# Kernel optimization log

Measured on AMD Instinct MI355X. Metric: run time of the kernel, lower is better.

## Reference

```python
import jax, jax.numpy as jnp
import numpy as np

N_NODES = 10000  # static number of graph nodes (segment count)


def setup_inputs() -> dict:
    key = jax.random.key(0)
    ks = jax.random.split(key, 7)
    B, N, DIN, DOUT, E = 2, N_NODES, 256, 256, 320000
    x = jax.random.normal(ks[0], (B, N, DIN), dtype=jnp.float32)
    W = jax.random.normal(ks[1], (DIN, DOUT), dtype=jnp.float32) * (1.0 / np.sqrt(DIN))
    loop_W = jax.random.normal(ks[2], (DIN, DOUT), dtype=jnp.float32) * (1.0 / np.sqrt(DIN))
    bias = jax.random.normal(ks[3], (DOUT,), dtype=jnp.float32) * 0.01
    edge_vals = jax.random.uniform(ks[4], (E,), dtype=jnp.float32)
    rows = jax.random.randint(ks[5], (E,), 0, N, dtype=jnp.int32)
    cols = jax.random.randint(ks[6], (E,), 0, N, dtype=jnp.int32)
    return {"x": x, "W": W, "loop_W": loop_W, "bias": bias,
            "edge_vals": edge_vals, "rows": rows, "cols": cols}


def reference(x, W, loop_W, bias, edge_vals, rows, cols):
    # Dense feature transforms: [b,n,din] @ [din,dout] -> [b,n,dout]
    support = jnp.einsum('bni,io->bno', x, W)
    support_loop = jnp.einsum('bni,io->bno', x, loop_W)
    # Sparse adjacency matmul (COO SpMM): out[r] += val_e * support[:, c_e, :]
    msgs = support[:, cols, :] * edge_vals[None, :, None]      # [b, E, dout]
    agg = jax.ops.segment_sum(
        jnp.swapaxes(msgs, 0, 1), rows, num_segments=N_NODES)   # [n, b, dout]
    agg = jnp.swapaxes(agg, 0, 1)                                # [b, n, dout]
    out = agg + support_loop + bias
    return jax.nn.relu(out)
```

## Files before the change

kernel.cpp:

```cpp
#include <hip/hip_runtime.h>
#include <hip/hip_bf16.h>


#define NN 10000
#define DK 256
#define DO 256
#define MT 20000
#define SCAN_T 256
#define SCAN_C 40

typedef short short8 __attribute__((ext_vector_type(8)));
typedef float f32x4 __attribute__((ext_vector_type(4)));

__device__ inline unsigned short f2bf(float f) {
    unsigned int u = __float_as_uint(f);
    u = (u + 0x7FFFu + ((u >> 16) & 1u)) >> 16;
    return (unsigned short)u;
}
__device__ inline float bf2f(unsigned short s) {
    return __uint_as_float(((unsigned int)s) << 16);
}

__global__ __launch_bounds__(256) void cvt_x(
    const float* __restrict__ X, unsigned short* __restrict__ Xb, int n8)
{
    const int i = blockIdx.x * 256 + threadIdx.x;
    if (i >= n8) return;
    const float4 a = ((const float4*)X)[2 * i];
    const float4 b = ((const float4*)X)[2 * i + 1];
    short8 o;
    o[0] = (short)f2bf(a.x); o[1] = (short)f2bf(a.y);
    o[2] = (short)f2bf(a.z); o[3] = (short)f2bf(a.w);
    o[4] = (short)f2bf(b.x); o[5] = (short)f2bf(b.y);
    o[6] = (short)f2bf(b.z); o[7] = (short)f2bf(b.w);
    *(short8*)&Xb[(size_t)i * 8] = o;
}

__global__ __launch_bounds__(256) void transpose_w(
    const float* __restrict__ W, const float* __restrict__ LW,
    unsigned short* __restrict__ Wt, unsigned short* __restrict__ LWt)
{
    __shared__ float tile[64][65];
    const float* src = blockIdx.z ? LW : W;
    unsigned short* dst = blockIdx.z ? LWt : Wt;
    const int k0 = blockIdx.x * 64, c0 = blockIdx.y * 64;
    #pragma unroll
    for (int it = 0; it < 16; ++it) {
        const int u = it * 256 + threadIdx.x;
        const int i = u >> 6, j = u & 63;
        tile[i][j] = src[(size_t)(k0 + i) * DO + c0 + j];
    }
    __syncthreads();
    #pragma unroll
    for (int it = 0; it < 16; ++it) {
        const int u = it * 256 + threadIdx.x;
        const int j = u >> 6, i = u & 63;
        dst[(size_t)(c0 + j) * DK + k0 + i] = f2bf(tile[i][j]);
    }
}

__global__ __launch_bounds__(256) void gemm_mfma(
    const unsigned short* __restrict__ Xb, const unsigned short* __restrict__ Wt,
    const unsigned short* __restrict__ LWt, const float* __restrict__ bias,
    unsigned short* __restrict__ sup, float* __restrict__ outv)
{
    __shared__ unsigned short As[8][128][8];
    __shared__ unsigned short Bs[8][128][8];
    const int t = threadIdx.x;
    const int wid = t >> 6, lane = t & 63;
    const int wm = wid >> 1, wn = wid & 1;
    const int m0 = blockIdx.x * 128;
    const int n0 = blockIdx.y * 128;
    const bool isLoop = (blockIdx.z != 0);
    const unsigned short* Bsrc = isLoop ? LWt : Wt;

    f32x4 acc[4][4];
    #pragma unroll
    for (int i = 0; i < 4; ++i)
        #pragma unroll
        for (int j = 0; j < 4; ++j)
            acc[i][j] = (f32x4){0.f, 0.f, 0.f, 0.f};

    for (int k0 = 0; k0 < DK; k0 += 64) {
        #pragma unroll
        for (int it = 0; it < 4; ++it) {
            const int u = it * 256 + t;
            const int row = u >> 3, kg = u & 7;
            const int grow = m0 + row;
            short8 v = (short8){0,0,0,0,0,0,0,0};
            if (grow < MT) v = *(const short8*)&Xb[(size_t)grow * DK + k0 + kg * 8];
            *(short8*)&As[kg][row ^ kg][0] = v;
        }
        #pragma unroll
        for (int it = 0; it < 4; ++it) {
            const int u = it * 256 + t;
            const int col = u >> 3, kg = u & 7;
            const short8 v = *(const short8*)&Bsrc[(size_t)(n0 + col) * DK + k0 + kg * 8];
            *(short8*)&Bs[kg][col ^ kg][0] = v;
        }
        __syncthreads();
        #pragma unroll
        for (int s = 0; s < 2; ++s) {
            const int kg = s * 4 + (lane >> 4);
            short8 af[4], bfv[4];
            #pragma unroll
            for (int i = 0; i < 4; ++i) {
                const int row = wm * 64 + i * 16 + (lane & 15);
                af[i] = *(const short8*)&As[kg][row ^ kg][0];
            }
            #pragma unroll
            for (int j = 0; j < 4; ++j) {
                const int col = wn * 64 + j * 16 + (lane & 15);
                bfv[j] = *(const short8*)&Bs[kg][col ^ kg][0];
            }
            #pragma unroll
            for (int i = 0; i < 4; ++i)
                #pragma unroll
                for (int j = 0; j < 4; ++j)
                    acc[i][j] = __builtin_amdgcn_mfma_f32_16x16x32_bf16(
                        af[i], bfv[j], acc[i][j], 0, 0, 0);
        }
        __syncthreads();
    }

    const int rbase = m0 + wm * 64;
    const int cbase = n0 + wn * 64;
    if (!isLoop) {
        #pragma unroll
        for (int i = 0; i < 4; ++i)
            #pragma unroll
            for (int q = 0; q < 4; ++q) {
                const int row = rbase + i * 16 + (lane >> 4) * 4 + q;
                if (row < MT) {
                    #pragma unroll
                    for (int j = 0; j < 4; ++j) {
                        const int col = cbase + j * 16 + (lane & 15);
                        sup[(size_t)row * DO + col] = f2bf(acc[i][j][q]);
                    }
                }
            }
    } else {
        #pragma unroll
        for (int i = 0; i < 4; ++i)
            #pragma unroll
            for (int q = 0; q < 4; ++q) {
                const int row = rbase + i * 16 + (lane >> 4) * 4 + q;
                if (row < MT) {
                    #pragma unroll
                    for (int j = 0; j < 4; ++j) {
                        const int col = cbase + j * 16 + (lane & 15);
                        outv[(size_t)row * DO + col] = acc[i][j][q] + bias[col];
                    }
                }
            }
    }
}

__global__ __launch_bounds__(256) void zero_counts(int* __restrict__ counts, int n)
{
    const int i = blockIdx.x * 256 + threadIdx.x;
    if (i < n) counts[i] = 0;
}

__global__ __launch_bounds__(256) void hist_rows(
    const int* __restrict__ rows, int* __restrict__ counts, int E)
{
    const int e = blockIdx.x * 256 + threadIdx.x;
    if (e < E) atomicAdd(&counts[rows[e]], 1);
}

__global__ __launch_bounds__(SCAN_T) void scan_rows(
    const int* __restrict__ counts, int* __restrict__ offsets,
    int* __restrict__ cursor)
{
    __shared__ int sums[SCAN_T];
    const int t = threadIdx.x;
    int local[SCAN_C];
    int s = 0;
    const int base = t * SCAN_C;
    #pragma unroll
    for (int i = 0; i < SCAN_C; ++i) {
        const int idx = base + i;
        const int c = (idx < NN) ? counts[idx] : 0;
        local[i] = s;
        s += c;
    }
    sums[t] = s;
    __syncthreads();
    for (int off = 1; off < SCAN_T; off <<= 1) {
        int u = (t >= off) ? sums[t - off] : 0;
        __syncthreads();
        sums[t] += u;
        __syncthreads();
    }
    const int excl = (t == 0) ? 0 : sums[t - 1];
    #pragma unroll
    for (int i = 0; i < SCAN_C; ++i) {
        const int idx = base + i;
        if (idx < NN) {
            const int o = excl + local[i];
            offsets[idx] = o;
            cursor[idx]  = o;
        }
    }
}

__global__ __launch_bounds__(256) void scatter_edges(
    const int* __restrict__ rows, const int* __restrict__ cols,
    const float* __restrict__ vals, int* __restrict__ cursor,
    float2* __restrict__ epack, int E)
{
    const int e = blockIdx.x * 256 + threadIdx.x;
    if (e >= E) return;
    const int p = atomicAdd(&cursor[rows[e]], 1);
    epack[p] = make_float2(__int_as_float(cols[e]), vals[e]);
}

__global__ __launch_bounds__(256) void agg_relu(
    const unsigned short* __restrict__ sup, const float2* __restrict__ epack,
    const int* __restrict__ offsets, const int* __restrict__ counts,
    float* __restrict__ outv)
{
    const int widx = (blockIdx.x * 256 + threadIdx.x) >> 6;
    if (widx >= 2 * NN) return;
    const int lane = threadIdx.x & 63;
    const int b = widx & 1, r = widx >> 1;
    const int d = lane * 4;
    const size_t supb = (size_t)b * NN * DO + d;
    const int start = offsets[r];
    const int deg   = counts[r];

    float a0 = 0.f, a1 = 0.f, a2 = 0.f, a3 = 0.f;
    #pragma unroll 4
    for (int i = 0; i < deg; ++i) {
        const float2 ep = epack[start + i];
        const int col = __float_as_int(ep.x);
        const float v = ep.y;
        const ushort4 s = *(const ushort4*)&sup[supb + (size_t)col * DO];
        a0 += v * bf2f(s.x); a1 += v * bf2f(s.y);
        a2 += v * bf2f(s.z); a3 += v * bf2f(s.w);
    }

    float* o = &outv[((size_t)b * NN + r) * DO + d];
    float4 t4 = *(const float4*)o;
    t4.x = fmaxf(t4.x + a0, 0.f); t4.y = fmaxf(t4.y + a1, 0.f);
    t4.z = fmaxf(t4.z + a2, 0.f); t4.w = fmaxf(t4.w + a3, 0.f);
    *(float4*)o = t4;
}

extern "C" void kernel_launch(void* const* d_in, const int* in_sizes, int n_in,
                              void* d_out, int out_size, void* d_ws, size_t ws_size,
                              hipStream_t stream)
{
    const float* x    = (const float*)d_in[0];
    const float* W    = (const float*)d_in[1];
    const float* LW   = (const float*)d_in[2];
    const float* bias = (const float*)d_in[3];
    const float* ev   = (const float*)d_in[4];
    const int*   rows = (const int*)d_in[5];
    const int*   cols = (const int*)d_in[6];
    float* out = (float*)d_out;

    const int E = in_sizes[4];

    char* wsb = (char*)d_ws;
    unsigned short* Xb    = (unsigned short*)wsb;
    float2*         epack = (float2*)wsb;
    unsigned short* Wt    = (unsigned short*)(wsb + 10240000);
    unsigned short* LWt   = (unsigned short*)(wsb + 10371072);
    unsigned short* supb  = (unsigned short*)(wsb + 10502144);
    int* counts  = (int*)(wsb + 20742144);
    int* offsets = (int*)(wsb + 20782144);
    int* cursor  = (int*)(wsb + 20822144);

    cvt_x<<<(MT * DK / 8 + 255) / 256, 256, 0, stream>>>(x, Xb, MT * DK / 8);
    transpose_w<<<dim3(4, 4, 2), 256, 0, stream>>>(W, LW, Wt, LWt);

    zero_counts<<<(NN + 255) / 256, 256, 0, stream>>>(counts, NN);
    hist_rows<<<(E + 255) / 256, 256, 0, stream>>>(rows, counts, E);
    scan_rows<<<1, SCAN_T, 0, stream>>>(counts, offsets, cursor);

    gemm_mfma<<<dim3((MT + 127) / 128, DO / 128, 2), 256, 0, stream>>>(
        Xb, Wt, LWt, bias, supb, out);

    scatter_edges<<<(E + 255) / 256, 256, 0, stream>>>(rows, cols, ev, cursor, epack, E);

    const int aggBlocks = (2 * NN * 64 + 255) / 256;
    agg_relu<<<aggBlocks, 256, 0, stream>>>(supb, epack, offsets, counts, out);
}
```

Baseline: 134.0 us.

## Fuse x conversion into GEMM and compute both weight products per block

Removes the separate fp32-to-bf16 conversion kernel by converting x tiles inside the GEMM load loop. Each GEMM block now computes both W and loop_W products from one shared A tile, which halves A traffic and the grid size but doubles accumulator registers. The zeroing of counts is folded into transpose_w, the scan uses 1024 threads, and the aggregation loop unroll is raised to 8. The extra registers may lower occupancy, and with half as many blocks the GEMM grid is smaller.

After: 149.5 us. 11.6% more time.

```diff
diff --git a/kernel.cpp b/kernel.cpp
--- a/kernel.cpp
+++ b/kernel.cpp
@@ -6,8 +6,8 @@
 #define DK 256
 #define DO 256
 #define MT 20000
-#define SCAN_T 256
-#define SCAN_C 40
+#define SCAN_T 1024
+#define SCAN_C 10
 
 typedef short short8 __attribute__((ext_vector_type(8)));
 typedef float f32x4 __attribute__((ext_vector_type(4)));
@@ -21,29 +21,26 @@
     return __uint_as_float(((unsigned int)s) << 16);
 }
 
-__global__ __launch_bounds__(256) void cvt_x(
-    const float* __restrict__ X, unsigned short* __restrict__ Xb, int n8)
-{
-    const int i = blockIdx.x * 256 + threadIdx.x;
-    if (i >= n8) return;
-    const float4 a = ((const float4*)X)[2 * i];
-    const float4 b = ((const float4*)X)[2 * i + 1];
-    short8 o;
-    o[0] = (short)f2bf(a.x); o[1] = (short)f2bf(a.y);
-    o[2] = (short)f2bf(a.z); o[3] = (short)f2bf(a.w);
-    o[4] = (short)f2bf(b.x); o[5] = (short)f2bf(b.y);
-    o[6] = (short)f2bf(b.z); o[7] = (short)f2bf(b.w);
-    *(short8*)&Xb[(size_t)i * 8] = o;
-}
-
 __global__ __launch_bounds__(256) void transpose_w(
     const float* __restrict__ W, const float* __restrict__ LW,
-    unsigned short* __restrict__ Wt, unsigned short* __restrict__ LWt)
+    unsigned short* __restrict__ Wt, unsigned short* __restrict__ LWt,
+    int* __restrict__ counts)
 {
     __shared__ float tile[64][65];
     const float* src = blockIdx.z ? LW : W;
     unsigned short* dst = blockIdx.z ? LWt : Wt;
     const int k0 = blockIdx.x * 64, c0 = blockIdx.y * 64;
+
+    if (blockIdx.z == 0) {
+        const int bid = blockIdx.x * 4 + blockIdx.y;
+        const int i = bid * 256 * 3 + threadIdx.x;
+        #pragma unroll
+        for (int q = 0; q < 3; ++q) {
+            const int idx = i + q * 256;
+            if (idx < NN) counts[idx] = 0;
+        }
+    }
+
     #pragma unroll
     for (int it = 0; it < 16; ++it) {
         const int u = it * 256 + threadIdx.x;
@@ -59,27 +56,28 @@
     }
 }
 
-__global__ __launch_bounds__(256) void gemm_mfma(
-    const unsigned short* __restrict__ Xb, const unsigned short* __restrict__ Wt,
+__global__ __launch_bounds__(256) void gemm_fused(
+    const float* __restrict__ X, const unsigned short* __restrict__ Wt,
     const unsigned short* __restrict__ LWt, const float* __restrict__ bias,
     unsigned short* __restrict__ sup, float* __restrict__ outv)
 {
     __shared__ unsigned short As[8][128][8];
-    __shared__ unsigned short Bs[8][128][8];
+    __shared__ unsigned short BsW[8][128][8];
+    __shared__ unsigned short BsL[8][128][8];
     const int t = threadIdx.x;
     const int wid = t >> 6, lane = t & 63;
     const int wm = wid >> 1, wn = wid & 1;
     const int m0 = blockIdx.x * 128;
     const int n0 = blockIdx.y * 128;
-    const bool isLoop = (blockIdx.z != 0);
-    const unsigned short* Bsrc = isLoop ? LWt : Wt;
-
-    f32x4 acc[4][4];
+
+    f32x4 accW[4][4], accL[4][4];
     #pragma unroll
     for (int i = 0; i < 4; ++i)
         #pragma unroll
-        for (int j = 0; j < 4; ++j)
-            acc[i][j] = (f32x4){0.f, 0.f, 0.f, 0.f};
+        for (int j = 0; j < 4; ++j) {
+            accW[i][j] = (f32x4){0.f, 0.f, 0.f, 0.f};
+            accL[i][j] = (f32x4){0.f, 0.f, 0.f, 0.f};
+        }
 
     for (int k0 = 0; k0 < DK; k0 += 64) {
         #pragma unroll
@@ -88,21 +86,29 @@
             const int row = u >> 3, kg = u & 7;
             const int grow = m0 + row;
             short8 v = (short8){0,0,0,0,0,0,0,0};
-            if (grow < MT) v = *(const short8*)&Xb[(size_t)grow * DK + k0 + kg * 8];
+            if (grow < MT) {
+                const float4 a = *(const float4*)&X[(size_t)grow * DK + k0 + kg * 8];
+                const float4 b = *(const float4*)&X[(size_t)grow * DK + k0 + kg * 8 + 4];
+                v[0] = (short)f2bf(a.x); v[1] = (short)f2bf(a.y);
+                v[2] = (short)f2bf(a.z); v[3] = (short)f2bf(a.w);
+                v[4] = (short)f2bf(b.x); v[5] = (short)f2bf(b.y);
+                v[6] = (short)f2bf(b.z); v[7] = (short)f2bf(b.w);
+            }
             *(short8*)&As[kg][row ^ kg][0] = v;
         }
         #pragma unroll
         for (int it = 0; it < 4; ++it) {
             const int u = it * 256 + t;
             const int col = u >> 3, kg = u & 7;
-            const short8 v = *(const short8*)&Bsrc[(size_t)(n0 + col) * DK + k0 + kg * 8];
-            *(short8*)&Bs[kg][col ^ kg][0] = v;
+            const size_t off = (size_t)(n0 + col) * DK + k0 + kg * 8;
+            *(short8*)&BsW[kg][col ^ kg][0] = *(const short8*)&Wt[off];
+            *(short8*)&BsL[kg][col ^ kg][0] = *(const short8*)&LWt[off];
         }
         __syncthreads();
         #pragma unroll
         for (int s = 0; s < 2; ++s) {
             const int kg = s * 4 + (lane >> 4);
-            short8 af[4], bfv[4];
+            short8 af[4], bW[4], bL[4];
             #pragma unroll
             for (int i = 0; i < 4; ++i) {
                 const int row = wm * 64 + i * 16 + (lane & 15);
@@ -111,55 +117,38 @@
             #pragma unroll
             for (int j = 0; j < 4; ++j) {
                 const int col = wn * 64 + j * 16 + (lane & 15);
-                bfv[j] = *(const short8*)&Bs[kg][col ^ kg][0];
+                bW[j] = *(const short8*)&BsW[kg][col ^ kg][0];
+                bL[j] = *(const short8*)&BsL[kg][col ^ kg][0];
             }
             #pragma unroll
             for (int i = 0; i < 4; ++i)
                 #pragma unroll
-                for (int j = 0; j < 4; ++j)
-                    acc[i][j] = __builtin_amdgcn_mfma_f32_16x16x32_bf16(
-                        af[i], bfv[j], acc[i][j], 0, 0, 0);
+                for (int j = 0; j < 4; ++j) {
+                    accW[i][j] = __builtin_amdgcn_mfma_f32_16x16x32_bf16(
+                        af[i], bW[j], accW[i][j], 0, 0, 0);
+                    accL[i][j] = __builtin_amdgcn_mfma_f32_16x16x32_bf16(
+                        af[i], bL[j], accL[i][j], 0, 0, 0);
+                }
         }
         __syncthreads();
     }
 
     const int rbase = m0 + wm * 64;
     const int cbase = n0 + wn * 64;
-    if (!isLoop) {
-        #pragma unroll
-        for (int i = 0; i < 4; ++i)
-            #pragma unroll
-            for (int q = 0; q < 4; ++q) {
-                const int row = rbase + i * 16 + (lane >> 4) * 4 + q;
-                if (row < MT) {
-                    #pragma unroll
-                    for (int j = 0; j < 4; ++j) {
-                        const int col = cbase + j * 16 + (lane & 15);
-                        sup[(size_t)row * DO + col] = f2bf(acc[i][j][q]);
-                    }
+    #pragma unroll
+    for (int i = 0; i < 4; ++i)
+        #pragma unroll
+        for (int q = 0; q < 4; ++q) {
+            const int row = rbase + i * 16 + (lane >> 4) * 4 + q;
+            if (row < MT) {
+                #pragma unroll
+                for (int j = 0; j < 4; ++j) {
+                    const int col = cbase + j * 16 + (lane & 15);
+                    sup[(size_t)row * DO + col] = f2bf(accW[i][j][q]);
+                    outv[(size_t)row * DO + col] = accL[i][j][q] + bias[col];
                 }
             }
-    } else {
-        #pragma unroll
-        for (int i = 0; i < 4; ++i)
-            #pragma unroll
-            for (int q = 0; q < 4; ++q) {
-                const int row = rbase + i * 16 + (lane >> 4) * 4 + q;
-                if (row < MT) {
-                    #pragma unroll
-                    for (int j = 0; j < 4; ++j) {
-                        const int col = cbase + j * 16 + (lane & 15);
-                        outv[(size_t)row * DO + col] = acc[i][j][q] + bias[col];
-                    }
-                }
-            }
-    }
-}
-
-__global__ __launch_bounds__(256) void zero_counts(int* __restrict__ counts, int n)
-{
-    const int i = blockIdx.x * 256 + threadIdx.x;
-    if (i < n) counts[i] = 0;
+        }
 }
 
 __global__ __launch_bounds__(256) void hist_rows(
@@ -231,7 +220,7 @@
     const int deg   = counts[r];
 
     float a0 = 0.f, a1 = 0.f, a2 = 0.f, a3 = 0.f;
-    #pragma unroll 4
+    #pragma unroll 8
     for (int i = 0; i < deg; ++i) {
         const float2 ep = epack[start + i];
         const int col = __float_as_int(ep.x);
@@ -264,24 +253,20 @@
     const int E = in_sizes[4];
 
     char* wsb = (char*)d_ws;
-    unsigned short* Xb    = (unsigned short*)wsb;
-    float2*         epack = (float2*)wsb;
-    unsigned short* Wt    = (unsigned short*)(wsb + 10240000);
-    unsigned short* LWt   = (unsigned short*)(wsb + 10371072);
-    unsigned short* supb  = (unsigned short*)(wsb + 10502144);
-    int* counts  = (int*)(wsb + 20742144);
-    int* offsets = (int*)(wsb + 20782144);
-    int* cursor  = (int*)(wsb + 20822144);
-
-    cvt_x<<<(MT * DK / 8 + 255) / 256, 256, 0, stream>>>(x, Xb, MT * DK / 8);
-    transpose_w<<<dim3(4, 4, 2), 256, 0, stream>>>(W, LW, Wt, LWt);
-
-    zero_counts<<<(NN + 255) / 256, 256, 0, stream>>>(counts, NN);
+    unsigned short* Wt    = (unsigned short*)wsb;
+    unsigned short* LWt   = (unsigned short*)(wsb + 131072);
+    unsigned short* supb  = (unsigned short*)(wsb + 262144);
+    int* counts  = (int*)(wsb + 10502144);
+    int* offsets = (int*)(wsb + 10542144);
+    int* cursor  = (int*)(wsb + 10582144);
+    float2* epack = (float2*)(wsb + 10622144);
+
+    transpose_w<<<dim3(4, 4, 2), 256, 0, stream>>>(W, LW, Wt, LWt, counts);
     hist_rows<<<(E + 255) / 256, 256, 0, stream>>>(rows, counts, E);
     scan_rows<<<1, SCAN_T, 0, stream>>>(counts, offsets, cursor);
 
-    gemm_mfma<<<dim3((MT + 127) / 128, DO / 128, 2), 256, 0, stream>>>(
-        Xb, Wt, LWt, bias, supb, out);
+    gemm_fused<<<dim3((MT + 127) / 128, DO / 128), 256, 0, stream>>>(
+        x, Wt, LWt, bias, supb, out);
 
     scatter_edges<<<(E + 255) / 256, 256, 0, stream>>>(rows, cols, ev, cursor, epack, E);
 
```
